# Optimization experiments

Hardware: AMD Instinct MI355X
Metric: run time of the kernel (lower is better)

## Reference

```python
import jax, jax.numpy as jnp
import numpy as np

N_NODES = 50000
N_EDGES = 800000
F_IN = 128


def setup_inputs() -> dict:
    key = jax.random.key(0)
    ks = jax.random.split(key, 8)
    x = jax.random.normal(ks[0], (N_NODES, F_IN), dtype=jnp.float32)
    edge_index = jax.random.randint(ks[1], (2, N_EDGES), 0, N_NODES, dtype=jnp.int64)
    def lin(k, fan_in, fan_out):
        bound = 1.0 / np.sqrt(fan_in)
        return jax.random.uniform(k, (fan_in, fan_out), jnp.float32, -bound, bound)
    W1 = lin(ks[2], F_IN, 64)
    W2 = lin(ks[3], 64, 64)
    W3 = lin(ks[4], 64, 64)
    Wf1 = lin(ks[5], 64, 32)
    Wf2 = lin(ks[6], 32, 1)
    return {
        'x': x, 'edge_index': edge_index,
        'W1': W1, 'b1': jnp.zeros((64,), jnp.float32),
        'W2': W2, 'b2': jnp.zeros((64,), jnp.float32),
        'W3': W3, 'b3': jnp.zeros((64,), jnp.float32),
        'Wf1': Wf1, 'bf1': jnp.zeros((32,), jnp.float32),
        'Wf2': Wf2, 'bf2': jnp.zeros((1,), jnp.float32),
    }


def reference(x, edge_index, W1, b1, W2, b2, W3, b3, Wf1, bf1, Wf2, bf2):
    row, col = edge_index[0], edge_index[1]
    for W, b in ((W1, b1), (W2, b2), (W3, b3)):
        agg = jax.ops.segment_sum(x[col], row, num_segments=N_NODES)  # [N, d]
        x = jax.nn.relu(agg @ W + b)
    h = x.mean(axis=0)                      # [64] global mean pool
    h = jax.nn.relu(h @ Wf1 + bf1)          # [32]
    out = jax.nn.sigmoid(h @ Wf2 + bf2)     # [1]
    return out
```

## Files before the change

### kernel.cpp

```cpp
#include <hip/hip_runtime.h>
#include <hip/hip_bf16.h>
#include <math.h>

#define N_NODES 50000
#define N_EDGES 800000
#define CAP 64
#define PAD_ROW 65535

typedef float v2f __attribute__((ext_vector_type(2)));

__device__ __forceinline__ unsigned int pack4_fp8(float f0, float f1,
                                                  float f2, float f3) {
    unsigned int p = 0;
    p = __builtin_amdgcn_cvt_pk_fp8_f32(f0, f1, p, false);
    p = __builtin_amdgcn_cvt_pk_fp8_f32(f2, f3, p, true);
    return p;
}

__device__ __forceinline__ float fp8_lo(unsigned int b) {
    const v2f t = __builtin_amdgcn_cvt_pk_f32_fp8(b, false);
    return t.x;
}

__global__ __launch_bounds__(256) void gemm_build(
    const float* __restrict__ in, const float* __restrict__ W,
    unsigned int* __restrict__ out8, int N,
    const int* __restrict__ rowv, const int* __restrict__ colv,
    int* __restrict__ cnt, unsigned short* __restrict__ buck, int E,
    int gemmGrid)
{
    __shared__ float Wl[128 * 64];
    __shared__ float xs[32][128];

    const int bid = blockIdx.x;
    const int grp = bid / 3;
    const int rem = bid - grp * 3;
    const int tid = threadIdx.x;

    if (rem != 0) {
        const int widx = grp * 2 + (rem - 1);
        const int e = widx * 256 + tid;
        if (e < E) {
            const int r = rowv[e];
            const int slot = atomicAdd(&cnt[r], 1);
            if (slot < CAP) buck[r * CAP + slot] = (unsigned short)colv[e];
        }
        return;
    }

    if (grp >= gemmGrid) return;
    const int j    = tid & 63;
    const int rq   = tid >> 6;
    const int base = grp * 32;

    for (int i = tid; i < 128 * 64; i += 256) Wl[i] = W[i];

    for (int i = tid; i < 32 * 128; i += 256) {
        const int r = i >> 7;
        const int k = i & 127;
        float v = 0.f;
        if (base + r < N) v = in[(size_t)(base + r) * 128 + k];
        xs[r][k] = v;
    }
    __syncthreads();

    float acc[8];
#pragma unroll
    for (int rr = 0; rr < 8; ++rr) acc[rr] = 0.f;

    for (int k = 0; k < 128; k += 4) {
        const float wv0 = Wl[(k + 0) * 64 + j];
        const float wv1 = Wl[(k + 1) * 64 + j];
        const float wv2 = Wl[(k + 2) * 64 + j];
        const float wv3 = Wl[(k + 3) * 64 + j];
#pragma unroll
        for (int rr = 0; rr < 8; ++rr) {
            const float4 xv = *(const float4*)&xs[rq + rr * 4][k];
            acc[rr] += xv.x * wv0 + xv.y * wv1 + xv.z * wv2 + xv.w * wv3;
        }
    }

    __syncthreads();
#pragma unroll
    for (int rr = 0; rr < 8; ++rr) xs[rq + rr * 4][j] = acc[rr];
    __syncthreads();
#pragma unroll
    for (int m = 0; m < 2; ++m) {
        const int idx = m * 256 + tid;
        const int r2 = idx >> 4;
        const int c4 = idx & 15;
        const int row = base + r2;
        if (row < N) {
            const unsigned int p = pack4_fp8(
                xs[r2][c4 * 4 + 0], xs[r2][c4 * 4 + 1],
                xs[r2][c4 * 4 + 2], xs[r2][c4 * 4 + 3]);
            out8[(size_t)row * 16 + c4] = p;
        }
    }
}

__global__ __launch_bounds__(256) void gemm_act64(
    const float* __restrict__ agg, const float* __restrict__ W,
    const float* __restrict__ bias, unsigned int* __restrict__ out8, int N)
{
    __shared__ float Wl[64 * 64];
    __shared__ float xs[32][64];

    const int tid = threadIdx.x;
    const int j   = tid & 63;
    const int rq  = tid >> 6;
    const int base = blockIdx.x * 32;

    for (int i = tid; i < 64 * 64; i += 256) Wl[i] = W[i];

    for (int i = tid; i < 32 * 64; i += 256) {
        const int r = i >> 6;
        const int k = i & 63;
        float v = 0.f;
        if (base + r < N) v = fmaxf(agg[(size_t)(base + r) * 64 + k] + bias[k], 0.f);
        xs[r][k] = v;
    }
    __syncthreads();

    float acc[8];
#pragma unroll
    for (int rr = 0; rr < 8; ++rr) acc[rr] = 0.f;

    for (int k = 0; k < 64; k += 4) {
        const float wv0 = Wl[(k + 0) * 64 + j];
        const float wv1 = Wl[(k + 1) * 64 + j];
        const float wv2 = Wl[(k + 2) * 64 + j];
        const float wv3 = Wl[(k + 3) * 64 + j];
#pragma unroll
        for (int rr = 0; rr < 8; ++rr) {
            const float4 xv = *(const float4*)&xs[rq + rr * 4][k];
            acc[rr] += xv.x * wv0 + xv.y * wv1 + xv.z * wv2 + xv.w * wv3;
        }
    }

    __syncthreads();
#pragma unroll
    for (int rr = 0; rr < 8; ++rr) xs[rq + rr * 4][j] = acc[rr];
    __syncthreads();
#pragma unroll
    for (int m = 0; m < 2; ++m) {
        const int idx = m * 256 + tid;
        const int r2 = idx >> 4;
        const int c4 = idx & 15;
        const int row = base + r2;
        if (row < N) {
            const unsigned int p = pack4_fp8(
                xs[r2][c4 * 4 + 0], xs[r2][c4 * 4 + 1],
                xs[r2][c4 * 4 + 2], xs[r2][c4 * 4 + 3]);
            out8[(size_t)row * 16 + c4] = p;
        }
    }
}

__device__ __forceinline__ float gather16(
    const unsigned char* __restrict__ y8b, int bval, int lane, const int base)
{
    float s0 = 0.f, s1 = 0.f, s2 = 0.f, s3 = 0.f;
#pragma unroll
    for (int k = 0; k < 16; k += 4) {
        const int c0 = __builtin_amdgcn_readlane(bval, base + k + 0);
        const int c1 = __builtin_amdgcn_readlane(bval, base + k + 1);
        const int c2 = __builtin_amdgcn_readlane(bval, base + k + 2);
        const int c3 = __builtin_amdgcn_readlane(bval, base + k + 3);
        const unsigned int b0 = y8b[(size_t)c0 * 64 + lane];
        const unsigned int b1 = y8b[(size_t)c1 * 64 + lane];
        const unsigned int b2 = y8b[(size_t)c2 * 64 + lane];
        const unsigned int b3 = y8b[(size_t)c3 * 64 + lane];
        s0 += fp8_lo(b0);
        s1 += fp8_lo(b1);
        s2 += fp8_lo(b2);
        s3 += fp8_lo(b3);
    }
    return (s0 + s1) + (s2 + s3);
}

__device__ __forceinline__ float node_accum(
    const unsigned char* __restrict__ y8b, const int* __restrict__ cnt,
    const unsigned short* __restrict__ buck, int n, int lane)
{
    int c0 = cnt[n]; if (c0 > CAP) c0 = CAP;
    const int bval = (int)buck[n * CAP + lane];
    float acc = 0.f;
    if (c0 > 0)  acc += gather16(y8b, bval, lane, 0);
    if (c0 > 16) acc += gather16(y8b, bval, lane, 16);
    if (c0 > 32) acc += gather16(y8b, bval, lane, 32);
    if (c0 > 48) acc += gather16(y8b, bval, lane, 48);
    return acc;
}

__global__ __launch_bounds__(256) void aggregate_b(
    const unsigned char* __restrict__ y8b, const int* __restrict__ cnt,
    const unsigned short* __restrict__ buck, float* __restrict__ agg, int N)
{
    const int w    = threadIdx.x >> 6;
    const int lane = threadIdx.x & 63;
    const int n = blockIdx.x * 4 + w;
    if (n >= N) return;
    const float acc = node_accum(y8b, cnt, buck, n, lane);
    agg[(size_t)n * 64 + lane] = acc;
}

__global__ __launch_bounds__(256) void agg_pool(
    const unsigned char* __restrict__ y8b, const int* __restrict__ cnt,
    const unsigned short* __restrict__ buck, const float* __restrict__ bias,
    float* __restrict__ hpart, int N)
{
    const int tid  = threadIdx.x;
    const int w    = tid >> 6;
    const int lane = tid & 63;
    const float b  = bias[lane];

    float s = 0.f;
    for (int n = blockIdx.x * 4 + w; n < N; n += gridDim.x * 4) {
        const float acc = node_accum(y8b, cnt, buck, n, lane);
        s += fmaxf(acc + b, 0.f);
    }

    __shared__ float red[4][64];
    red[w][lane] = s;
    __syncthreads();
    if (tid < 64) {
        const float t = red[0][tid] + red[1][tid] + red[2][tid] + red[3][tid];
        atomicAdd(&hpart[tid], t);
    }
}

__global__ __launch_bounds__(64) void head_kernel(
    const float* __restrict__ hpart, const float* __restrict__ Wf1,
    const float* __restrict__ bf1, const float* __restrict__ Wf2,
    const float* __restrict__ bf2, float* __restrict__ out, float invN)
{
    __shared__ float hm[64];
    __shared__ float t[32];
    const int tid = threadIdx.x;
    hm[tid] = hpart[tid] * invN;
    __syncthreads();
    if (tid < 32) {
        float a = bf1[tid];
        for (int k = 0; k < 64; ++k) a += hm[k] * Wf1[k * 32 + tid];
        t[tid] = fmaxf(a, 0.f);
    }
    __syncthreads();
    if (tid == 0) {
        float a = bf2[0];
        for (int i = 0; i < 32; ++i) a += t[i] * Wf2[i];
        out[0] = 1.f / (1.f + expf(-a));
    }
}

extern "C" void kernel_launch(void* const* d_in, const int* in_sizes, int n_in,
                              void* d_out, int out_size, void* d_ws, size_t ws_size,
                              hipStream_t stream)
{
    const float* x   = (const float*)d_in[0];
    const int*   ei  = (const int*)d_in[1];
    const float* W1  = (const float*)d_in[2];
    const float* b1  = (const float*)d_in[3];
    const float* W2  = (const float*)d_in[4];
    const float* b2  = (const float*)d_in[5];
    const float* W3  = (const float*)d_in[6];
    const float* b3  = (const float*)d_in[7];
    const float* Wf1 = (const float*)d_in[8];
    const float* bf1 = (const float*)d_in[9];
    const float* Wf2 = (const float*)d_in[10];
    const float* bf2 = (const float*)d_in[11];
    float* out = (float*)d_out;

    const int N = N_NODES;
    const int E = N_EDGES;
    const int* rowv = ei;
    const int* colv = ei + E;

    float*          aggf  = (float*)d_ws;
    unsigned char*  y8b   = (unsigned char*)(aggf + (size_t)N * 64);
    float*          hpart = (float*)(y8b + (size_t)65536 * 64);
    int*            cnt   = (int*)(hpart + 64);
    unsigned short* buck  = (unsigned short*)(cnt + N);

    const int gemmGrid = (N + 31) / 32;
    const int aggGrid  = (N + 3) / 4;

    hipMemsetAsync(cnt, 0, (size_t)N * sizeof(int), stream);
    hipMemsetAsync(buck, 0xFF, (size_t)N * CAP * sizeof(unsigned short), stream);
    hipMemsetAsync(y8b + (size_t)PAD_ROW * 64, 0, 64, stream);

    gemm_build<<<gemmGrid * 3, 256, 0, stream>>>(
        x, W1, (unsigned int*)y8b, N, rowv, colv, cnt, buck, E, gemmGrid);

    aggregate_b<<<aggGrid, 256, 0, stream>>>(y8b, cnt, buck, aggf, N);

    gemm_act64<<<gemmGrid, 256, 0, stream>>>(aggf, W2, b1, (unsigned int*)y8b, N);
    aggregate_b<<<aggGrid, 256, 0, stream>>>(y8b, cnt, buck, aggf, N);

    gemm_act64<<<gemmGrid, 256, 0, stream>>>(aggf, W3, b2, (unsigned int*)y8b, N);
    hipMemsetAsync(hpart, 0, 64 * sizeof(float), stream);
    agg_pool<<<1024, 256, 0, stream>>>(y8b, cnt, buck, b3, hpart, N);
    head_kernel<<<1, 64, 0, stream>>>(hpart, Wf1, bf1, Wf2, bf2, out,
                                      1.0f / (float)N);
}
```

Measured before the change: 261.7 us.

## Loop gather to exact neighbor count, drop padding memsets and LDS weight staging

```diff
diff --git a/kernel.cpp b/kernel.cpp
--- a/kernel.cpp
+++ b/kernel.cpp
@@ -5,7 +5,6 @@
 #define N_NODES 50000
 #define N_EDGES 800000
 #define CAP 64
-#define PAD_ROW 65535
 
 typedef float v2f __attribute__((ext_vector_type(2)));
 
@@ -29,7 +28,6 @@
     int* __restrict__ cnt, unsigned short* __restrict__ buck, int E,
     int gemmGrid)
 {
-    __shared__ float Wl[128 * 64];
     __shared__ float xs[32][128];
 
     const int bid = blockIdx.x;
@@ -53,8 +51,6 @@
     const int rq   = tid >> 6;
     const int base = grp * 32;
 
-    for (int i = tid; i < 128 * 64; i += 256) Wl[i] = W[i];
-
     for (int i = tid; i < 32 * 128; i += 256) {
         const int r = i >> 7;
         const int k = i & 127;
@@ -69,10 +65,10 @@
     for (int rr = 0; rr < 8; ++rr) acc[rr] = 0.f;
 
     for (int k = 0; k < 128; k += 4) {
-        const float wv0 = Wl[(k + 0) * 64 + j];
-        const float wv1 = Wl[(k + 1) * 64 + j];
-        const float wv2 = Wl[(k + 2) * 64 + j];
-        const float wv3 = Wl[(k + 3) * 64 + j];
+        const float wv0 = W[(k + 0) * 64 + j];
+        const float wv1 = W[(k + 1) * 64 + j];
+        const float wv2 = W[(k + 2) * 64 + j];
+        const float wv3 = W[(k + 3) * 64 + j];
 #pragma unroll
         for (int rr = 0; rr < 8; ++rr) {
             const float4 xv = *(const float4*)&xs[rq + rr * 4][k];
@@ -103,15 +99,12 @@
     const float* __restrict__ agg, const float* __restrict__ W,
     const float* __restrict__ bias, unsigned int* __restrict__ out8, int N)
 {
-    __shared__ float Wl[64 * 64];
     __shared__ float xs[32][64];
 
     const int tid = threadIdx.x;
     const int j   = tid & 63;
     const int rq  = tid >> 6;
     const int base = blockIdx.x * 32;
-
-    for (int i = tid; i < 64 * 64; i += 256) Wl[i] = W[i];
 
     for (int i = tid; i < 32 * 64; i += 256) {
         const int r = i >> 6;
@@ -127,10 +120,10 @@
     for (int rr = 0; rr < 8; ++rr) acc[rr] = 0.f;
 
     for (int k = 0; k < 64; k += 4) {
-        const float wv0 = Wl[(k + 0) * 64 + j];
-        const float wv1 = Wl[(k + 1) * 64 + j];
-        const float wv2 = Wl[(k + 2) * 64 + j];
-        const float wv3 = Wl[(k + 3) * 64 + j];
+        const float wv0 = W[(k + 0) * 64 + j];
+        const float wv1 = W[(k + 1) * 64 + j];
+        const float wv2 = W[(k + 2) * 64 + j];
+        const float wv3 = W[(k + 3) * 64 + j];
 #pragma unroll
         for (int rr = 0; rr < 8; ++rr) {
             const float4 xv = *(const float4*)&xs[rq + rr * 4][k];
@@ -157,40 +150,29 @@
     }
 }
 
-__device__ __forceinline__ float gather16(
-    const unsigned char* __restrict__ y8b, int bval, int lane, const int base)
-{
-    float s0 = 0.f, s1 = 0.f, s2 = 0.f, s3 = 0.f;
-#pragma unroll
-    for (int k = 0; k < 16; k += 4) {
-        const int c0 = __builtin_amdgcn_readlane(bval, base + k + 0);
-        const int c1 = __builtin_amdgcn_readlane(bval, base + k + 1);
-        const int c2 = __builtin_amdgcn_readlane(bval, base + k + 2);
-        const int c3 = __builtin_amdgcn_readlane(bval, base + k + 3);
-        const unsigned int b0 = y8b[(size_t)c0 * 64 + lane];
-        const unsigned int b1 = y8b[(size_t)c1 * 64 + lane];
-        const unsigned int b2 = y8b[(size_t)c2 * 64 + lane];
-        const unsigned int b3 = y8b[(size_t)c3 * 64 + lane];
-        s0 += fp8_lo(b0);
-        s1 += fp8_lo(b1);
-        s2 += fp8_lo(b2);
-        s3 += fp8_lo(b3);
-    }
-    return (s0 + s1) + (s2 + s3);
-}
-
 __device__ __forceinline__ float node_accum(
     const unsigned char* __restrict__ y8b, const int* __restrict__ cnt,
     const unsigned short* __restrict__ buck, int n, int lane)
 {
     int c0 = cnt[n]; if (c0 > CAP) c0 = CAP;
     const int bval = (int)buck[n * CAP + lane];
-    float acc = 0.f;
-    if (c0 > 0)  acc += gather16(y8b, bval, lane, 0);
-    if (c0 > 16) acc += gather16(y8b, bval, lane, 16);
-    if (c0 > 32) acc += gather16(y8b, bval, lane, 32);
-    if (c0 > 48) acc += gather16(y8b, bval, lane, 48);
-    return acc;
+    float s0 = 0.f, s1 = 0.f, s2 = 0.f, s3 = 0.f;
+    int i = 0;
+    for (; i + 4 <= c0; i += 4) {
+        const int a0 = __builtin_amdgcn_readlane(bval, i + 0);
+        const int a1 = __builtin_amdgcn_readlane(bval, i + 1);
+        const int a2 = __builtin_amdgcn_readlane(bval, i + 2);
+        const int a3 = __builtin_amdgcn_readlane(bval, i + 3);
+        s0 += fp8_lo(y8b[(size_t)a0 * 64 + lane]);
+        s1 += fp8_lo(y8b[(size_t)a1 * 64 + lane]);
+        s2 += fp8_lo(y8b[(size_t)a2 * 64 + lane]);
+        s3 += fp8_lo(y8b[(size_t)a3 * 64 + lane]);
+    }
+    for (; i < c0; ++i) {
+        const int a = __builtin_amdgcn_readlane(bval, i);
+        s0 += fp8_lo(y8b[(size_t)a * 64 + lane]);
+    }
+    return (s0 + s1) + (s2 + s3);
 }
 
 __global__ __launch_bounds__(256) void aggregate_b(
@@ -278,7 +260,7 @@
 
     float*          aggf  = (float*)d_ws;
     unsigned char*  y8b   = (unsigned char*)(aggf + (size_t)N * 64);
-    float*          hpart = (float*)(y8b + (size_t)65536 * 64);
+    float*          hpart = (float*)(y8b + (size_t)N * 64);
     int*            cnt   = (int*)(hpart + 64);
     unsigned short* buck  = (unsigned short*)(cnt + N);
 
@@ -286,8 +268,6 @@
     const int aggGrid  = (N + 3) / 4;
 
     hipMemsetAsync(cnt, 0, (size_t)N * sizeof(int), stream);
-    hipMemsetAsync(buck, 0xFF, (size_t)N * CAP * sizeof(unsigned short), stream);
-    hipMemsetAsync(y8b + (size_t)PAD_ROW * 64, 0, 64, stream);
 
     gemm_build<<<gemmGrid * 3, 256, 0, stream>>>(
         x, W1, (unsigned int*)y8b, N, rowv, colv, cnt, buck, E, gemmGrid);
```

Result: slower. 273.1 us (+4.4%).
